# Performance work log

Measured on AMD Instinct MI355X. Metric: run time of the kernel, lower is better.

## Reference

```python
import jax, jax.numpy as jnp
import numpy as np

E, N, G = 102400, 100000, 64
D_NODE, D_EDGE, D_GLOB, K = 256, 256, 128, 4
LAYERS = [512, 512, 256]
LN_EPS = 1e-3  # keras LayerNormalization default epsilon


def setup_inputs() -> dict:
    key = jax.random.key(0)
    ks = jax.random.split(key, 12)
    d_in = D_EDGE + K * D_NODE + D_GLOB  # 1408
    inp = {
        "feat": jax.random.normal(ks[0], (E, D_EDGE), jnp.float32),
        "nodes": jax.random.normal(ks[1], (N, D_NODE), jnp.float32),
        "gfeat": jax.random.normal(ks[2], (G, D_GLOB), jnp.float32),
        "ind": jax.random.randint(ks[3], (E, K), 0, N, jnp.int32),
        "num": jnp.full((G,), E // G, jnp.int32),  # sum(num) == E
    }
    dims = [d_in] + LAYERS
    for i in range(3):
        scale = 1.0 / np.sqrt(dims[i])
        inp[f"W{i+1}"] = jax.random.normal(ks[4 + i], (dims[i], dims[i + 1]), jnp.float32) * scale
        inp[f"b{i+1}"] = jnp.zeros((dims[i + 1],), jnp.float32)
    inp["gamma"] = jnp.ones((LAYERS[-1],), jnp.float32)
    inp["beta"] = jnp.zeros((LAYERS[-1],), jnp.float32)
    return inp


def reference(feat, nodes, gfeat, ind, num, W1, b1, W2, b2, W3, b3, gamma, beta):
    e = feat.shape[0]
    # _fixed_number_to_one: gather K nodes per hyperedge, flatten -> [E, K*D_NODE]
    gathered = nodes[ind].reshape(e, -1)
    # _one_to_segments: broadcast per-graph globals to their edges -> [E, D_GLOB]
    graph_ids = jnp.repeat(jnp.arange(num.shape[0]), num, total_repeat_length=e)
    glob = gfeat[graph_ids]
    x = jnp.concatenate([feat, gathered, glob], axis=1)  # [E, 1408]
    h = jax.nn.relu(x @ W1 + b1)
    h = jax.nn.relu(h @ W2 + b2)
    h = jax.nn.sigmoid(h @ W3 + b3)
    # keras LayerNormalization over the last axis
    mu = jnp.mean(h, axis=-1, keepdims=True)
    var = jnp.var(h, axis=-1, keepdims=True)
    return gamma * (h - mu) * jax.lax.rsqrt(var + LN_EPS) + beta
```

## Files before the change

### kernel.cpp

```cpp
#include <hip/hip_runtime.h>
#include <hip/hip_fp16.h>

#define E_EDGES 102400
#define N_NODES 100000
#define G_GRAPHS 64
#define D_EDGE 256
#define D_NODE 256
#define D_GLOB 128
#define KNB 4
#define D_IN 1408
#define H1D 512
#define H2D 512
#define H3D 256
#define LN_EPS 1e-3f

typedef _Float16 half8 __attribute__((ext_vector_type(8)));
typedef float f32x4 __attribute__((ext_vector_type(4)));

__device__ __forceinline__ void gload16(const void* g, void* l) {
    __builtin_amdgcn_global_load_lds((const __attribute__((address_space(1))) void*)g,
                                     (__attribute__((address_space(3))) void*)l, 16, 0, 0);
}


__global__ void k_prefix(const int* __restrict__ num, int* __restrict__ prefix) {
    if (threadIdx.x == 0) {
        int acc = 0;
        prefix[0] = 0;
        for (int g = 0; g < G_GRAPHS; ++g) { acc += num[g]; prefix[g + 1] = acc; }
    }
}

__global__ void k_gid(const int* __restrict__ prefix, int* __restrict__ gid) {
    int e = blockIdx.x * blockDim.x + threadIdx.x;
    if (e >= E_EDGES) return;
    int lo = 0, hi = G_GRAPHS;
    while (hi - lo > 1) {
        int mid = (lo + hi) >> 1;
        if (e >= prefix[mid]) lo = mid; else hi = mid;
    }
    gid[e] = lo;
}

__global__ void k_transpose(const float* __restrict__ src, _Float16* __restrict__ dst,
                            int Ks, int Ns) {
    long total = (long)Ks * Ns;
    for (long idx = (long)blockIdx.x * blockDim.x + threadIdx.x; idx < total;
         idx += (long)gridDim.x * blockDim.x) {
        int n = (int)(idx / Ks);
        int k = (int)(idx - (long)n * Ks);
        dst[idx] = (_Float16)src[(long)k * Ns + n];
    }
}

__global__ void k_cvt16(const float* __restrict__ src, _Float16* __restrict__ dst, long n8) {
    for (long i = (long)blockIdx.x * blockDim.x + threadIdx.x; i < n8;
         i += (long)gridDim.x * blockDim.x) {
        float4 u = reinterpret_cast<const float4*>(src)[i * 2];
        float4 v = reinterpret_cast<const float4*>(src)[i * 2 + 1];
        half8 h;
        h[0] = (_Float16)u.x; h[1] = (_Float16)u.y; h[2] = (_Float16)u.z; h[3] = (_Float16)u.w;
        h[4] = (_Float16)v.x; h[5] = (_Float16)v.y; h[6] = (_Float16)v.z; h[7] = (_Float16)v.w;
        reinterpret_cast<half8*>(dst)[i] = h;
    }
}


template <int KD, bool GATHER>
__global__ __launch_bounds__(512) void k_gemm_pipe(
    const _Float16* __restrict__ A,
    const _Float16* __restrict__ feat16, const _Float16* __restrict__ nodes16,
    const _Float16* __restrict__ gfeat16,
    const int* __restrict__ ind, const int* __restrict__ gid,
    const _Float16* __restrict__ Wt,
    const float* __restrict__ bias, _Float16* __restrict__ out) {
    constexpr int NT = KD / 64;
    __shared__ __align__(16) char lds[3 * 49152];

    const int t = threadIdx.x;
    const int bn = blockIdx.x, bm = blockIdx.y;
    const int n0 = bn * 256;
    const int w = t >> 6, lane = t & 63;
    const int wr = w >> 2, wc = w & 3;
    const int lr = lane & 15, lk = lane >> 4;

    const int srow = t >> 3;
    const int gslot = (t & 7) ^ (srow & 7);
    const int wbase = w * 8;

    int4 iv0, iv1;
    int g0 = 0, g1 = 0;
    int e0 = 0, e1 = 0;
    if constexpr (GATHER) {
        e0 = bm * 128 + srow;
        e1 = e0 + 64;
        iv0 = *reinterpret_cast<const int4*>(ind + (size_t)e0 * KNB);
        iv1 = *reinterpret_cast<const int4*>(ind + (size_t)e1 * KNB);
        g0 = gid[e0];
        g1 = gid[e1];
    }

    f32x4 acc[4][4];
#pragma unroll
    for (int m = 0; m < 4; m++)
#pragma unroll
        for (int n = 0; n < 4; n++) acc[m][n] = (f32x4)0.f;

    auto stage = [&](int kt, char* abuf, char* bbuf) {
#pragma unroll
        for (int c = 0; c < 2; ++c) {
            const _Float16* src;
            if constexpr (GATHER) {
                if (kt < 4) {
                    src = feat16 + (size_t)(c ? e1 : e0) * D_EDGE + kt * 64;
                } else if (kt < 20) {
                    int j = (kt - 4) >> 2;
                    int4 iv = c ? iv1 : iv0;
                    int nidx = j == 0 ? iv.x : j == 1 ? iv.y : j == 2 ? iv.z : iv.w;
                    src = nodes16 + (size_t)nidx * D_NODE + ((kt - 4) & 3) * 64;
                } else {
                    src = gfeat16 + (size_t)(c ? g1 : g0) * D_GLOB + (kt - 20) * 64;
                }
            } else {
                src = A + (size_t)(bm * 128 + c * 64 + srow) * KD + kt * 64;
            }
            gload16(src + gslot * 8, abuf + (c * 64 + wbase) * 128);
        }
#pragma unroll
        for (int c = 0; c < 4; ++c) {
            const _Float16* src = Wt + (size_t)(n0 + c * 64 + srow) * KD + kt * 64;
            gload16(src + gslot * 8, bbuf + (c * 64 + wbase) * 128);
        }
    };

    stage(0, lds, lds + 16384);
    stage(1, lds + 49152, lds + 49152 + 16384);
    asm volatile("s_waitcnt vmcnt(6)" ::: "memory");
    __builtin_amdgcn_s_barrier();

    int cur = 0;
    for (int kt = 0; kt < NT; ++kt) {
        const int pf = kt + 2;
        if (pf < NT) {
            const int pb = cur == 0 ? 2 : cur - 1;
            stage(pf, lds + pb * 49152, lds + pb * 49152 + 16384);
        }
        const char* ab = lds + cur * 49152;
        const char* bb = ab + 16384;
#pragma unroll
        for (int kk = 0; kk < 2; ++kk) {
            half8 a[4], b[4];
#pragma unroll
            for (int m = 0; m < 4; ++m) {
                int row = wr * 64 + m * 16 + lr;
                a[m] = *reinterpret_cast<const half8*>(
                    ab + row * 128 + ((((kk << 2) | lk)) ^ (lr & 7)) * 16);
            }
#pragma unroll
            for (int n = 0; n < 4; ++n) {
                int row = wc * 64 + n * 16 + lr;
                b[n] = *reinterpret_cast<const half8*>(
                    bb + row * 128 + ((((kk << 2) | lk)) ^ (lr & 7)) * 16);
            }
            __builtin_amdgcn_s_setprio(1);
#pragma unroll
            for (int m = 0; m < 4; ++m)
#pragma unroll
                for (int n = 0; n < 4; ++n)
                    acc[m][n] = __builtin_amdgcn_mfma_f32_16x16x32_f16(a[m], b[n], acc[m][n], 0, 0, 0);
            __builtin_amdgcn_s_setprio(0);
        }
        if (pf < NT) asm volatile("s_waitcnt vmcnt(6)" ::: "memory");
        else         asm volatile("s_waitcnt vmcnt(0)" ::: "memory");
        __builtin_amdgcn_s_barrier();
        cur = cur == 2 ? 0 : cur + 1;
    }

#pragma unroll
    for (int n = 0; n < 4; ++n) {
        int col = n0 + wc * 64 + n * 16 + lr;
        float bv = bias[col];
#pragma unroll
        for (int m = 0; m < 4; ++m) {
            int rbase = bm * 128 + wr * 64 + m * 16 + lk * 4;
#pragma unroll
            for (int q = 0; q < 4; ++q) {
                float v = acc[m][n][q] + bv;
                v = v > 0.f ? v : 0.f;
                out[(size_t)(rbase + q) * H1D + col] = (_Float16)v;
            }
        }
    }
}


__global__ __launch_bounds__(512) void k_gemm3_ln(
    const _Float16* __restrict__ A, const _Float16* __restrict__ Wt,
    const float* __restrict__ bias, const float* __restrict__ gamma,
    const float* __restrict__ beta, float* __restrict__ out) {
    __shared__ __align__(16) _Float16 As[128][64];
    __shared__ __align__(16) _Float16 Bs[256][64];
    __shared__ float red1[128][4];
    __shared__ float red2[128][4];
    __shared__ float mvmu[128];
    __shared__ float mvrs[128];
    const int t = threadIdx.x;
    const int bm = blockIdx.x;
    const int w = t >> 6, lane = t & 63;
    const int wr = w >> 2, wc = w & 3, lr = lane & 15, lk = lane >> 4;

    const int srow = w * 8 + (lane >> 3);
    const int scol = (lane & 7) * 8;
    const _Float16* Ab = A + (size_t)(bm * 128 + srow) * H2D + scol;
    const _Float16* Bb = Wt + (size_t)srow * H2D + scol;

    f32x4 acc[4][4];
#pragma unroll
    for (int m = 0; m < 4; m++)
#pragma unroll
        for (int n = 0; n < 4; n++) acc[m][n] = (f32x4)0.f;

    for (int kt = 0; kt < 8; ++kt) {
        const int k0 = kt * 64;
        __syncthreads();
#pragma unroll
        for (int i = 0; i < 2; i++)
            gload16(Ab + (size_t)i * 64 * H2D + k0, (char*)As + i * 8192 + w * 1024);
#pragma unroll
        for (int i = 0; i < 4; i++)
            gload16(Bb + (size_t)i * 64 * H2D + k0, (char*)Bs + i * 8192 + w * 1024);
        __syncthreads();
#pragma unroll
        for (int kk = 0; kk < 2; kk++) {
            half8 a[4], b[4];
#pragma unroll
            for (int m = 0; m < 4; m++)
                a[m] = *reinterpret_cast<half8*>(&As[wr * 64 + m * 16 + lr][kk * 32 + lk * 8]);
#pragma unroll
            for (int n = 0; n < 4; n++)
                b[n] = *reinterpret_cast<half8*>(&Bs[wc * 64 + n * 16 + lr][kk * 32 + lk * 8]);
#pragma unroll
            for (int m = 0; m < 4; m++)
#pragma unroll
                for (int n = 0; n < 4; n++)
                    acc[m][n] = __builtin_amdgcn_mfma_f32_16x16x32_f16(a[m], b[n], acc[m][n], 0, 0, 0);
        }
    }

#pragma unroll
    for (int n = 0; n < 4; n++) {
        int col = wc * 64 + n * 16 + lr;
        float bv = bias[col];
#pragma unroll
        for (int m = 0; m < 4; m++)
#pragma unroll
            for (int q = 0; q < 4; q++) {
                float x = acc[m][n][q] + bv;
                acc[m][n][q] = 1.f / (1.f + __expf(-x));
            }
    }

#pragma unroll
    for (int m = 0; m < 4; m++)
#pragma unroll
        for (int q = 0; q < 4; q++) {
            float s1 = 0.f, s2 = 0.f;
#pragma unroll
            for (int n = 0; n < 4; n++) {
                float x = acc[m][n][q];
                s1 += x; s2 += x * x;
            }
            s1 += __shfl_xor(s1, 1); s2 += __shfl_xor(s2, 1);
            s1 += __shfl_xor(s1, 2); s2 += __shfl_xor(s2, 2);
            s1 += __shfl_xor(s1, 4); s2 += __shfl_xor(s2, 4);
            s1 += __shfl_xor(s1, 8); s2 += __shfl_xor(s2, 8);
            if (lr == 0) {
                int row = wr * 64 + m * 16 + lk * 4 + q;
                red1[row][wc] = s1;
                red2[row][wc] = s2;
            }
        }
    __syncthreads();
    if (t < 128) {
        float s = red1[t][0] + red1[t][1] + red1[t][2] + red1[t][3];
        float ss = red2[t][0] + red2[t][1] + red2[t][2] + red2[t][3];
        float mu = s * (1.f / H3D);
        float var = ss * (1.f / H3D) - mu * mu;
        mvmu[t] = mu;
        mvrs[t] = rsqrtf(var + LN_EPS);
    }
    __syncthreads();
#pragma unroll
    for (int m = 0; m < 4; m++)
#pragma unroll
        for (int q = 0; q < 4; q++) {
            int row = wr * 64 + m * 16 + lk * 4 + q;
            float mu = mvmu[row], rs = mvrs[row];
#pragma unroll
            for (int n = 0; n < 4; n++) {
                int col = wc * 64 + n * 16 + lr;
                out[(size_t)(bm * 128 + row) * H3D + col] =
                    gamma[col] * (acc[m][n][q] - mu) * rs + beta[col];
            }
        }
}


extern "C" void kernel_launch(void* const* d_in, const int* in_sizes, int n_in,
                              void* d_out, int out_size, void* d_ws, size_t ws_size,
                              hipStream_t stream) {
    const float* feat  = (const float*)d_in[0];
    const float* nodes = (const float*)d_in[1];
    const float* gfeat = (const float*)d_in[2];
    const int*   ind   = (const int*)d_in[3];
    const int*   num   = (const int*)d_in[4];
    const float* W1    = (const float*)d_in[5];
    const float* b1    = (const float*)d_in[6];
    const float* W2    = (const float*)d_in[7];
    const float* b2    = (const float*)d_in[8];
    const float* W3    = (const float*)d_in[9];
    const float* b3    = (const float*)d_in[10];
    const float* gamma = (const float*)d_in[11];
    const float* beta  = (const float*)d_in[12];
    float* out = (float*)d_out;

    char* ws = (char*)d_ws;
    size_t off = 0;
    auto alloc = [&](size_t bytes) {
        size_t o = off;
        off += (bytes + 255) & ~(size_t)255;
        return o;
    };
    int* prefix       = (int*)(ws + alloc((G_GRAPHS + 1) * sizeof(int)));
    int* gid          = (int*)(ws + alloc((size_t)E_EDGES * sizeof(int)));
    _Float16* W1t     = (_Float16*)(ws + alloc((size_t)H1D * D_IN * 2));
    _Float16* W2t     = (_Float16*)(ws + alloc((size_t)H2D * H1D * 2));
    _Float16* W3t     = (_Float16*)(ws + alloc((size_t)H3D * H2D * 2));
    _Float16* feat16  = (_Float16*)(ws + alloc((size_t)E_EDGES * D_EDGE * 2));
    _Float16* nodes16 = (_Float16*)(ws + alloc((size_t)N_NODES * D_NODE * 2));
    _Float16* gfeat16 = (_Float16*)(ws + alloc((size_t)G_GRAPHS * D_GLOB * 2));
    _Float16* h1      = (_Float16*)(ws + alloc((size_t)E_EDGES * H1D * 2));
    _Float16* h2      = (_Float16*)(ws + alloc((size_t)E_EDGES * H2D * 2));
    (void)ws_size; (void)in_sizes; (void)n_in; (void)out_size;

    k_prefix<<<1, 64, 0, stream>>>(num, prefix);
    k_gid<<<(E_EDGES + 255) / 256, 256, 0, stream>>>(prefix, gid);
    k_cvt16<<<2048, 256, 0, stream>>>(feat, feat16, (long)E_EDGES * D_EDGE / 8);
    k_cvt16<<<2048, 256, 0, stream>>>(nodes, nodes16, (long)N_NODES * D_NODE / 8);
    k_cvt16<<<16, 256, 0, stream>>>(gfeat, gfeat16, (long)G_GRAPHS * D_GLOB / 8);
    k_transpose<<<1024, 256, 0, stream>>>(W1, W1t, D_IN, H1D);
    k_transpose<<<512, 256, 0, stream>>>(W2, W2t, H1D, H2D);
    k_transpose<<<256, 256, 0, stream>>>(W3, W3t, H2D, H3D);
    k_gemm_pipe<D_IN, true><<<dim3(H1D / 256, E_EDGES / 128), 512, 0, stream>>>(
        nullptr, feat16, nodes16, gfeat16, ind, gid, W1t, b1, h1);
    k_gemm_pipe<H1D, false><<<dim3(H2D / 256, E_EDGES / 128), 512, 0, stream>>>(
        h1, nullptr, nullptr, nullptr, nullptr, nullptr, W2t, b2, h2);
    k_gemm3_ln<<<E_EDGES / 128, 512, 0, stream>>>(h2, W3t, b3, gamma, beta, out);
}
```

Measured before the change: 629.9 us.

## Merge preprocessing kernels, tile weight transpose, and triple-buffer the third GEMM

Folds the prefix and graph-id kernels into one, merges the three fp32-to-fp16 conversions into a single launch, and replaces the strided per-element weight transposes with one LDS-tiled transpose kernel that covers all three matrices. The last GEMM with LayerNorm now uses the same triple-buffered async-LDS pipeline as the earlier GEMMs, with an XOR-swizzled LDS layout and MFMA priority hints. The aim is to cut launch overhead, uncoalesced transpose traffic, and load stalls in the final GEMM. The cost is higher LDS use (about 147KB) in the final kernel, which may limit occupancy.

```diff
diff --git a/kernel.cpp b/kernel.cpp
--- a/kernel.cpp
+++ b/kernel.cpp
@@ -23,45 +23,70 @@
 }
 
 
-__global__ void k_prefix(const int* __restrict__ num, int* __restrict__ prefix) {
+__global__ void k_gid2(const int* __restrict__ num, int* __restrict__ gid) {
+    __shared__ int pfx[G_GRAPHS + 1];
     if (threadIdx.x == 0) {
-        int acc = 0;
-        prefix[0] = 0;
-        for (int g = 0; g < G_GRAPHS; ++g) { acc += num[g]; prefix[g + 1] = acc; }
-    }
-}
-
-__global__ void k_gid(const int* __restrict__ prefix, int* __restrict__ gid) {
+        int a = 0;
+        pfx[0] = 0;
+        for (int g = 0; g < G_GRAPHS; ++g) { a += num[g]; pfx[g + 1] = a; }
+    }
+    __syncthreads();
     int e = blockIdx.x * blockDim.x + threadIdx.x;
     if (e >= E_EDGES) return;
     int lo = 0, hi = G_GRAPHS;
     while (hi - lo > 1) {
         int mid = (lo + hi) >> 1;
-        if (e >= prefix[mid]) lo = mid; else hi = mid;
+        if (e >= pfx[mid]) lo = mid; else hi = mid;
     }
     gid[e] = lo;
 }
 
-__global__ void k_transpose(const float* __restrict__ src, _Float16* __restrict__ dst,
-                            int Ks, int Ns) {
-    long total = (long)Ks * Ns;
-    for (long idx = (long)blockIdx.x * blockDim.x + threadIdx.x; idx < total;
-         idx += (long)gridDim.x * blockDim.x) {
-        int n = (int)(idx / Ks);
-        int k = (int)(idx - (long)n * Ks);
-        dst[idx] = (_Float16)src[(long)k * Ns + n];
-    }
-}
-
-__global__ void k_cvt16(const float* __restrict__ src, _Float16* __restrict__ dst, long n8) {
-    for (long i = (long)blockIdx.x * blockDim.x + threadIdx.x; i < n8;
+__global__ void k_cvtall(const float* __restrict__ feat, const float* __restrict__ nodes,
+                         const float* __restrict__ gfeat,
+                         _Float16* __restrict__ feat16, _Float16* __restrict__ nodes16,
+                         _Float16* __restrict__ gfeat16) {
+    const long c1 = (long)E_EDGES * D_EDGE / 8;
+    const long c2 = c1 + (long)N_NODES * D_NODE / 8;
+    const long c3 = c2 + (long)G_GRAPHS * D_GLOB / 8;
+    for (long i = (long)blockIdx.x * blockDim.x + threadIdx.x; i < c3;
          i += (long)gridDim.x * blockDim.x) {
-        float4 u = reinterpret_cast<const float4*>(src)[i * 2];
-        float4 v = reinterpret_cast<const float4*>(src)[i * 2 + 1];
+        const float* s;
+        _Float16* d;
+        long j;
+        if (i < c1)      { s = feat;  d = feat16;  j = i; }
+        else if (i < c2) { s = nodes; d = nodes16; j = i - c1; }
+        else             { s = gfeat; d = gfeat16; j = i - c2; }
+        float4 u = reinterpret_cast<const float4*>(s)[j * 2];
+        float4 v = reinterpret_cast<const float4*>(s)[j * 2 + 1];
         half8 h;
         h[0] = (_Float16)u.x; h[1] = (_Float16)u.y; h[2] = (_Float16)u.z; h[3] = (_Float16)u.w;
         h[4] = (_Float16)v.x; h[5] = (_Float16)v.y; h[6] = (_Float16)v.z; h[7] = (_Float16)v.w;
-        reinterpret_cast<half8*>(dst)[i] = h;
+        reinterpret_cast<half8*>(d)[j] = h;
+    }
+}
+
+__global__ __launch_bounds__(256) void k_wt(
+    const float* __restrict__ W1, const float* __restrict__ W2, const float* __restrict__ W3,
+    _Float16* __restrict__ W1t, _Float16* __restrict__ W2t, _Float16* __restrict__ W3t) {
+    __shared__ float tile[64][65];
+    int b = blockIdx.x;
+    const float* src;
+    _Float16* dst;
+    int Ks, Ns, kt, nt;
+    if (b < 176)      { src = W1; dst = W1t; Ks = D_IN; Ns = H1D; kt = b >> 3; nt = b & 7; }
+    else if (b < 240) { b -= 176; src = W2; dst = W2t; Ks = H1D; Ns = H2D; kt = b >> 3; nt = b & 7; }
+    else              { b -= 240; src = W3; dst = W3t; Ks = H2D; Ns = H3D; kt = b >> 2; nt = b & 3; }
+    const int tx = threadIdx.x & 63, ty = threadIdx.x >> 6;
+#pragma unroll
+    for (int r = 0; r < 16; ++r) {
+        int k = ty * 16 + r;
+        tile[k][tx] = src[(size_t)(kt * 64 + k) * Ns + nt * 64 + tx];
+    }
+    __syncthreads();
+#pragma unroll
+    for (int r = 0; r < 16; ++r) {
+        int n = ty * 16 + r;
+        dst[(size_t)(nt * 64 + n) * Ks + kt * 64 + tx] = (_Float16)tile[tx][n];
     }
 }
 
@@ -194,25 +219,26 @@
 }
 
 
-__global__ __launch_bounds__(512) void k_gemm3_ln(
+__global__ __launch_bounds__(512) void k_gemm3p(
     const _Float16* __restrict__ A, const _Float16* __restrict__ Wt,
     const float* __restrict__ bias, const float* __restrict__ gamma,
     const float* __restrict__ beta, float* __restrict__ out) {
-    __shared__ __align__(16) _Float16 As[128][64];
-    __shared__ __align__(16) _Float16 Bs[256][64];
+    constexpr int NT = H2D / 64;
+    __shared__ __align__(16) char lds[3 * 49152];
     __shared__ float red1[128][4];
     __shared__ float red2[128][4];
     __shared__ float mvmu[128];
     __shared__ float mvrs[128];
+
     const int t = threadIdx.x;
     const int bm = blockIdx.x;
     const int w = t >> 6, lane = t & 63;
-    const int wr = w >> 2, wc = w & 3, lr = lane & 15, lk = lane >> 4;
-
-    const int srow = w * 8 + (lane >> 3);
-    const int scol = (lane & 7) * 8;
-    const _Float16* Ab = A + (size_t)(bm * 128 + srow) * H2D + scol;
-    const _Float16* Bb = Wt + (size_t)srow * H2D + scol;
+    const int wr = w >> 2, wc = w & 3;
+    const int lr = lane & 15, lk = lane >> 4;
+
+    const int srow = t >> 3;
+    const int gslot = (t & 7) ^ (srow & 7);
+    const int wbase = w * 8;
 
     f32x4 acc[4][4];
 #pragma unroll
@@ -220,31 +246,60 @@
 #pragma unroll
         for (int n = 0; n < 4; n++) acc[m][n] = (f32x4)0.f;
 
-    for (int kt = 0; kt < 8; ++kt) {
-        const int k0 = kt * 64;
-        __syncthreads();
-#pragma unroll
-        for (int i = 0; i < 2; i++)
-            gload16(Ab + (size_t)i * 64 * H2D + k0, (char*)As + i * 8192 + w * 1024);
-#pragma unroll
-        for (int i = 0; i < 4; i++)
-            gload16(Bb + (size_t)i * 64 * H2D + k0, (char*)Bs + i * 8192 + w * 1024);
-        __syncthreads();
-#pragma unroll
-        for (int kk = 0; kk < 2; kk++) {
+    auto stage = [&](int kt, char* abuf, char* bbuf) {
+#pragma unroll
+        for (int c = 0; c < 2; ++c) {
+            const _Float16* src = A + (size_t)(bm * 128 + c * 64 + srow) * H2D + kt * 64;
+            gload16(src + gslot * 8, abuf + (c * 64 + wbase) * 128);
+        }
+#pragma unroll
+        for (int c = 0; c < 4; ++c) {
+            const _Float16* src = Wt + (size_t)(c * 64 + srow) * H2D + kt * 64;
+            gload16(src + gslot * 8, bbuf + (c * 64 + wbase) * 128);
+        }
+    };
+
+    stage(0, lds, lds + 16384);
+    stage(1, lds + 49152, lds + 49152 + 16384);
+    asm volatile("s_waitcnt vmcnt(6)" ::: "memory");
+    __builtin_amdgcn_s_barrier();
+
+    int cur = 0;
+    for (int kt = 0; kt < NT; ++kt) {
+        const int pf = kt + 2;
+        if (pf < NT) {
+            const int pb = cur == 0 ? 2 : cur - 1;
+            stage(pf, lds + pb * 49152, lds + pb * 49152 + 16384);
+        }
+        const char* ab = lds + cur * 49152;
+        const char* bb = ab + 16384;
+#pragma unroll
+        for (int kk = 0; kk < 2; ++kk) {
             half8 a[4], b[4];
 #pragma unroll
-            for (int m = 0; m < 4; m++)
-                a[m] = *reinterpret_cast<half8*>(&As[wr * 64 + m * 16 + lr][kk * 32 + lk * 8]);
-#pragma unroll
-            for (int n = 0; n < 4; n++)
-                b[n] = *reinterpret_cast<half8*>(&Bs[wc * 64 + n * 16 + lr][kk * 32 + lk * 8]);
-#pragma unroll
-            for (int m = 0; m < 4; m++)
-#pragma unroll
-                for (int n = 0; n < 4; n++)
+            for (int m = 0; m < 4; ++m) {
+                int row = wr * 64 + m * 16 + lr;
+                a[m] = *reinterpret_cast<const half8*>(
+                    ab + row * 128 + ((((kk << 2) | lk)) ^ (lr & 7)) * 16);
+            }
+#pragma unroll
+            for (int n = 0; n < 4; ++n) {
+                int row = wc * 64 + n * 16 + lr;
+                b[n] = *reinterpret_cast<const half8*>(
+                    bb + row * 128 + ((((kk << 2) | lk)) ^ (lr & 7)) * 16);
+            }
+            __builtin_amdgcn_s_setprio(1);
+#pragma unroll
+            for (int m = 0; m < 4; ++m)
+#pragma unroll
+                for (int n = 0; n < 4; ++n)
                     acc[m][n] = __builtin_amdgcn_mfma_f32_16x16x32_f16(a[m], b[n], acc[m][n], 0, 0, 0);
-        }
+            __builtin_amdgcn_s_setprio(0);
+        }
+        if (pf < NT) asm volatile("s_waitcnt vmcnt(6)" ::: "memory");
+        else         asm volatile("s_waitcnt vmcnt(0)" ::: "memory");
+        __builtin_amdgcn_s_barrier();
+        cur = cur == 2 ? 0 : cur + 1;
     }
 
 #pragma unroll
@@ -331,7 +386,6 @@
         off += (bytes + 255) & ~(size_t)255;
         return o;
     };
-    int* prefix       = (int*)(ws + alloc((G_GRAPHS + 1) * sizeof(int)));
     int* gid          = (int*)(ws + alloc((size_t)E_EDGES * sizeof(int)));
     _Float16* W1t     = (_Float16*)(ws + alloc((size_t)H1D * D_IN * 2));
     _Float16* W2t     = (_Float16*)(ws + alloc((size_t)H2D * H1D * 2));
@@ -343,17 +397,12 @@
     _Float16* h2      = (_Float16*)(ws + alloc((size_t)E_EDGES * H2D * 2));
     (void)ws_size; (void)in_sizes; (void)n_in; (void)out_size;
 
-    k_prefix<<<1, 64, 0, stream>>>(num, prefix);
-    k_gid<<<(E_EDGES + 255) / 256, 256, 0, stream>>>(prefix, gid);
-    k_cvt16<<<2048, 256, 0, stream>>>(feat, feat16, (long)E_EDGES * D_EDGE / 8);
-    k_cvt16<<<2048, 256, 0, stream>>>(nodes, nodes16, (long)N_NODES * D_NODE / 8);
-    k_cvt16<<<16, 256, 0, stream>>>(gfeat, gfeat16, (long)G_GRAPHS * D_GLOB / 8);
-    k_transpose<<<1024, 256, 0, stream>>>(W1, W1t, D_IN, H1D);
-    k_transpose<<<512, 256, 0, stream>>>(W2, W2t, H1D, H2D);
-    k_transpose<<<256, 256, 0, stream>>>(W3, W3t, H2D, H3D);
+    k_gid2<<<(E_EDGES + 255) / 256, 256, 0, stream>>>(num, gid);
+    k_cvtall<<<2048, 256, 0, stream>>>(feat, nodes, gfeat, feat16, nodes16, gfeat16);
+    k_wt<<<272, 256, 0, stream>>>(W1, W2, W3, W1t, W2t, W3t);
     k_gemm_pipe<D_IN, true><<<dim3(H1D / 256, E_EDGES / 128), 512, 0, stream>>>(
         nullptr, feat16, nodes16, gfeat16, ind, gid, W1t, b1, h1);
     k_gemm_pipe<H1D, false><<<dim3(H2D / 256, E_EDGES / 128), 512, 0, stream>>>(
         h1, nullptr, nullptr, nullptr, nullptr, nullptr, W2t, b2, h2);
-    k_gemm3_ln<<<E_EDGES / 128, 512, 0, stream>>>(h2, W3t, b3, gamma, beta, out);
-}
+    k_gemm3p<<<E_EDGES / 128, 512, 0, stream>>>(h2, W3t, b3, gamma, beta, out);
+}
```

Measured after the change: 632.4 us. About the same (+0.4%).
